# Performance work log

Hardware: AMD Instinct MI355X
Metric: run time of the kernel (lower is better)

## Reference

```python
import jax, jax.numpy as jnp
import numpy as np

D_MODEL = 768
N_HEADS = 4          # n_kv_heads
D_HEAD = 64          # d_model // n_heads = 768 // 12
DIM = N_HEADS * D_HEAD  # 256


def _feature_map(x):
    # ELU + 1 kernel approximation
    return jax.nn.elu(x) + 1.0


def setup_inputs() -> dict:
    key = jax.random.key(0)
    ks = jax.random.split(key, 6)
    B, T = 2, 4096
    s_in = 1.0 / np.sqrt(D_MODEL)
    s_out = 1.0 / np.sqrt(DIM)
    return {
        "x": jax.random.normal(ks[0], (B, T, D_MODEL), dtype=jnp.float32),
        "Wq": jax.random.normal(ks[1], (D_MODEL, DIM), dtype=jnp.float32) * s_in,
        "Wk": jax.random.normal(ks[2], (D_MODEL, DIM), dtype=jnp.float32) * s_in,
        "Wv": jax.random.normal(ks[3], (D_MODEL, DIM), dtype=jnp.float32) * s_in,
        "Wo": jax.random.normal(ks[4], (DIM, D_MODEL), dtype=jnp.float32) * s_out,
        "Wg": jax.random.normal(ks[5], (D_MODEL, D_MODEL), dtype=jnp.float32) * s_in,
    }


def reference(x, Wq, Wk, Wv, Wo, Wg):
    B, T, _ = x.shape
    H, D = N_HEADS, D_HEAD
    # projections -> (B, H, T, D)
    q = (x @ Wq).reshape(B, T, H, D).transpose(0, 2, 1, 3)
    k = (x @ Wk).reshape(B, T, H, D).transpose(0, 2, 1, 3)
    v = (x @ Wv).reshape(B, T, H, D).transpose(0, 2, 1, 3)
    q = _feature_map(q)
    k = _feature_map(k)
    # causal linear attention: running kv outer-product state, cumsum over T
    kv_cum = jnp.cumsum(jnp.einsum('bhte,bhtd->bhtde', k, v), axis=2)  # (B,H,T,D,D)
    z_cum = jnp.cumsum(k, axis=2)                                      # (B,H,T,D)
    out = jnp.einsum('bhte,bhted->bhtd', q, kv_cum)
    denom = jnp.maximum(jnp.einsum('bhte,bhte->bht', q, z_cum), 1e-6)[..., None]
    out = (out / denom).transpose(0, 2, 1, 3).reshape(B, T, H * D)
    gate = jax.nn.sigmoid(x @ Wg)
    return (out @ Wo) * gate
```

## Files before the change

kernel.cpp:

```cpp
#include <hip/hip_runtime.h>
#include <math.h>

#define BATCH 2
#define TSEQ 4096
#define DM 768
#define HEADS 4
#define DHEAD 64
#define DIMQ 256
#define MROWS (BATCH*TSEQ)
#define CHUNK 64
#define NCHUNK (TSEQ/CHUNK)
#define STATE (DHEAD*DHEAD + DHEAD)
#define KSPLIT (DM*2)
#define KS2 (DIMQ*2)

typedef __attribute__((ext_vector_type(8))) short bf16x8;
typedef __attribute__((ext_vector_type(4))) float f32x4;

__device__ __forceinline__ float act_elu1(float x){ return x > 0.f ? x + 1.f : expf(x); }
__device__ __forceinline__ float act_sig(float x){ return 1.f/(1.f + expf(-x)); }

__device__ __forceinline__ void fma4(float4& o, float a, const float4& b){
    o.x = fmaf(a, b.x, o.x); o.y = fmaf(a, b.y, o.y);
    o.z = fmaf(a, b.z, o.z); o.w = fmaf(a, b.w, o.w);
}
__device__ __forceinline__ float comp4(const float4& v, int u){
    return u==0 ? v.x : u==1 ? v.y : u==2 ? v.z : v.w;
}

__device__ __forceinline__ unsigned short bf16_rne(float f){
    unsigned u = __float_as_uint(f);
    u += 0x7FFFu + ((u >> 16) & 1u);
    return (unsigned short)(u >> 16);
}

__device__ __forceinline__ void gload_lds16(const void* g, void* l){
    __builtin_amdgcn_global_load_lds(
        (const __attribute__((address_space(1))) unsigned char*)g,
        (__attribute__((address_space(3))) unsigned char*)l, 16, 0, 0);
}

__global__ __launch_bounds__(192)
void split_x(const float* __restrict__ x, unsigned short* __restrict__ xs)
{
    const int r = blockIdx.x;
    const int c = threadIdx.x * 4;
    float4 v = *(const float4*)&x[(size_t)r*DM + c];
    float vv[4] = {v.x, v.y, v.z, v.w};
    unsigned short h[4], l[4];
    #pragma unroll
    for (int j = 0; j < 4; j++){
        h[j] = bf16_rne(vv[j]);
        float hf = __uint_as_float((unsigned)h[j] << 16);
        l[j] = bf16_rne(vv[j] - hf);
    }
    ushort4 h4 = {h[0],h[1],h[2],h[3]}, l4 = {l[0],l[1],l[2],l[3]};
    *(ushort4*)&xs[(size_t)r*KSPLIT + c] = h4;
    *(ushort4*)&xs[(size_t)r*KSPLIT + DM + c] = l4;
}

__global__ __launch_bounds__(256)
void split_w(const float* __restrict__ Wq, const float* __restrict__ Wk,
             const float* __restrict__ Wv, const float* __restrict__ Wg,
             unsigned short* __restrict__ wt)
{
    const int n0 = blockIdx.x * 64;
    const int k0 = blockIdx.y * 64;
    const float* W; int ldw, c0;
    if      (n0 < 256) { W = Wq; ldw = DIMQ; c0 = n0;       }
    else if (n0 < 512) { W = Wk; ldw = DIMQ; c0 = n0 - 256; }
    else if (n0 < 768) { W = Wv; ldw = DIMQ; c0 = n0 - 512; }
    else               { W = Wg; ldw = DM;   c0 = n0 - 768; }

    __shared__ float T[64][65];
    const int t = threadIdx.x;
    const int lr = t >> 4, lc = (t & 15) * 4;
    #pragma unroll
    for (int i = 0; i < 4; i++){
        int r = lr + i*16;
        float4 v = *(const float4*)&W[(size_t)(k0+r)*ldw + c0 + lc];
        T[r][lc+0]=v.x; T[r][lc+1]=v.y; T[r][lc+2]=v.z; T[r][lc+3]=v.w;
    }
    __syncthreads();
    const int rn = t >> 2, kc = (t & 3) * 16;
    unsigned short hb[16], lb[16];
    #pragma unroll
    for (int j = 0; j < 16; j++){
        float f = T[kc+j][rn];
        hb[j] = bf16_rne(f);
        float hf = __uint_as_float((unsigned)hb[j] << 16);
        lb[j] = bf16_rne(f - hf);
    }
    size_t base = (size_t)(n0+rn)*KSPLIT + k0 + kc;
    #pragma unroll
    for (int q = 0; q < 4; q++){
        ushort4 hv = {hb[q*4],hb[q*4+1],hb[q*4+2],hb[q*4+3]};
        ushort4 lv = {lb[q*4],lb[q*4+1],lb[q*4+2],lb[q*4+3]};
        *(ushort4*)&wt[base + q*4] = hv;
        *(ushort4*)&wt[base + DM + q*4] = lv;
    }
}

__global__ __launch_bounds__(256)
void split_wo(const float* __restrict__ Wo, unsigned short* __restrict__ wot)
{
    const int n0 = blockIdx.x * 64;
    const int k0 = blockIdx.y * 64;
    __shared__ float T[64][65];
    const int t = threadIdx.x;
    const int lr = t >> 4, lc = (t & 15) * 4;
    #pragma unroll
    for (int i = 0; i < 4; i++){
        int r = lr + i*16;
        float4 v = *(const float4*)&Wo[(size_t)(k0+r)*DM + n0 + lc];
        T[r][lc+0]=v.x; T[r][lc+1]=v.y; T[r][lc+2]=v.z; T[r][lc+3]=v.w;
    }
    __syncthreads();
    const int rn = t >> 2, kc = (t & 3) * 16;
    unsigned short hb[16], lb[16];
    #pragma unroll
    for (int j = 0; j < 16; j++){
        float f = T[kc+j][rn];
        hb[j] = bf16_rne(f);
        float hf = __uint_as_float((unsigned)hb[j] << 16);
        lb[j] = bf16_rne(f - hf);
    }
    size_t base = (size_t)(n0+rn)*KS2 + k0 + kc;
    #pragma unroll
    for (int q = 0; q < 4; q++){
        ushort4 hv = {hb[q*4],hb[q*4+1],hb[q*4+2],hb[q*4+3]};
        ushort4 lv = {lb[q*4],lb[q*4+1],lb[q*4+2],lb[q*4+3]};
        *(ushort4*)&wot[base + q*4] = hv;
        *(ushort4*)&wot[base + DIMQ + q*4] = lv;
    }
}

__global__ __launch_bounds__(256, 2)
void gemm_qkvg_mfma(const unsigned short* __restrict__ xs,
                    const unsigned short* __restrict__ wt,
                    float* __restrict__ qws, float* __restrict__ kws,
                    float* __restrict__ vws, float* __restrict__ gws)
{
    __shared__ unsigned short Ah[128*32];
    __shared__ unsigned short Al[128*32];
    __shared__ unsigned short Bh[128*32];
    __shared__ unsigned short Bl[128*32];

    const int m0 = blockIdx.x * 128;
    const int n0 = blockIdx.y * 128;
    const int tid = threadIdx.x;
    const int lane = tid & 63, w = tid >> 6;
    const int wm = (w & 1) * 64, wn = (w >> 1) * 64;
    const int l15 = lane & 15, lq = lane >> 4;

    const int srow = tid >> 2, scq = tid & 3;
    const unsigned short* xr0 = xs + (size_t)(m0+srow)   * KSPLIT + scq*8;
    const unsigned short* xr1 = xs + (size_t)(m0+srow+64)* KSPLIT + scq*8;
    const unsigned short* br0 = wt + (size_t)(n0+srow)   * KSPLIT + scq*8;
    const unsigned short* br1 = wt + (size_t)(n0+srow+64)* KSPLIT + scq*8;

    f32x4 acc[4][4];
    #pragma unroll
    for (int i = 0; i < 4; i++)
        #pragma unroll
        for (int j = 0; j < 4; j++)
            acc[i][j] = (f32x4){0.f, 0.f, 0.f, 0.f};

    #pragma unroll 1
    for (int ks = 0; ks < 24; ks++){
        const int o = ks*32;
        __syncthreads();
        gload_lds16(xr0 + o,      &Ah[tid*8]);
        gload_lds16(xr1 + o,      &Ah[2048 + tid*8]);
        gload_lds16(xr0 + DM + o, &Al[tid*8]);
        gload_lds16(xr1 + DM + o, &Al[2048 + tid*8]);
        gload_lds16(br0 + o,      &Bh[tid*8]);
        gload_lds16(br1 + o,      &Bh[2048 + tid*8]);
        gload_lds16(br0 + DM + o, &Bl[tid*8]);
        gload_lds16(br1 + DM + o, &Bl[2048 + tid*8]);
        __syncthreads();

        bf16x8 ah[4], al[4], bh[4], bl[4];
        #pragma unroll
        for (int im = 0; im < 4; im++){
            ah[im] = *(const bf16x8*)&Ah[(wm + im*16 + l15)*32 + lq*8];
            al[im] = *(const bf16x8*)&Al[(wm + im*16 + l15)*32 + lq*8];
        }
        #pragma unroll
        for (int jn = 0; jn < 4; jn++){
            bh[jn] = *(const bf16x8*)&Bh[(wn + jn*16 + l15)*32 + lq*8];
            bl[jn] = *(const bf16x8*)&Bl[(wn + jn*16 + l15)*32 + lq*8];
        }
        #pragma unroll
        for (int im = 0; im < 4; im++)
            #pragma unroll
            for (int jn = 0; jn < 4; jn++){
                acc[im][jn] = __builtin_amdgcn_mfma_f32_16x16x32_bf16(
                    ah[im], bh[jn], acc[im][jn], 0, 0, 0);
                acc[im][jn] = __builtin_amdgcn_mfma_f32_16x16x32_bf16(
                    ah[im], bl[jn], acc[im][jn], 0, 0, 0);
                acc[im][jn] = __builtin_amdgcn_mfma_f32_16x16x32_bf16(
                    al[im], bh[jn], acc[im][jn], 0, 0, 0);
            }
    }

    float* dst; int ld, cb, mode;
    const int bj = blockIdx.y;
    if      (bj < 2) { dst = qws; ld = DIMQ; cb = bj*128;       mode = 1; }
    else if (bj < 4) { dst = kws; ld = DIMQ; cb = (bj-2)*128;   mode = 1; }
    else if (bj < 6) { dst = vws; ld = DIMQ; cb = (bj-4)*128;   mode = 0; }
    else             { dst = gws; ld = DM;   cb = (bj-6)*128;   mode = 2; }

    #pragma unroll
    for (int im = 0; im < 4; im++){
        const int rb = m0 + wm + im*16 + lq*4;
        #pragma unroll
        for (int jn = 0; jn < 4; jn++){
            const int col = cb + wn + jn*16 + l15;
            f32x4 a = acc[im][jn];
            #pragma unroll
            for (int r = 0; r < 4; r++){
                float v0 = a[r];
                float vv = (mode == 1) ? act_elu1(v0)
                         : (mode == 2) ? act_sig(v0) : v0;
                dst[(size_t)(rb + r)*ld + col] = vv;
            }
        }
    }
}

__global__ __launch_bounds__(256, 2)
void chunk_state(const float* __restrict__ kws, const float* __restrict__ vws,
                 float* __restrict__ Sws)
{
    __shared__ float Ks[64][64];
    __shared__ float Vt[64][68];

    const int blk = blockIdx.x;
    const int c = blk & (NCHUNK-1);
    const int bh = blk >> 6;
    const int b = bh >> 2, h = bh & 3;
    const int row0 = b*TSEQ + c*CHUNK;
    const int col0 = h*DHEAD;
    const int tid = threadIdx.x;

    #pragma unroll
    for (int i = 0; i < 4; i++) {
        int flat = tid + i*256;
        int s = flat >> 4, dq = flat & 15;
        float4 k4 = *(const float4*)&kws[(size_t)(row0+s)*DIMQ + col0 + dq*4];
        *(float4*)&Ks[s][dq*4] = k4;
        float4 v4 = *(const float4*)&vws[(size_t)(row0+s)*DIMQ + col0 + dq*4];
        Vt[dq*4+0][s] = v4.x; Vt[dq*4+1][s] = v4.y;
        Vt[dq*4+2][s] = v4.z; Vt[dq*4+3][s] = v4.w;
    }
    __syncthreads();

    const int e = tid >> 2, d0 = (tid & 3) * 16;
    float acc[16];
    #pragma unroll
    for (int j = 0; j < 16; j++) acc[j] = 0.f;
    for (int s = 0; s < 64; s++) {
        float ve = Vt[e][s];
        #pragma unroll
        for (int j = 0; j < 16; j++) acc[j] = fmaf(ve, Ks[s][d0+j], acc[j]);
    }
    float* Sp = Sws + (size_t)blk * STATE;
    #pragma unroll
    for (int j = 0; j < 16; j++) Sp[e*64 + d0 + j] = acc[j];

    if (tid < 64) {
        float z = 0.f;
        for (int s = 0; s < 64; s++) z += Ks[s][tid];
        Sp[4096 + tid] = z;
    }
}

__global__ __launch_bounds__(256)
void prefix_scan(const float* __restrict__ Sws, float* __restrict__ Pws)
{
    const int bh = blockIdx.x;
    const int i = blockIdx.y*256 + threadIdx.x;
    if (i >= STATE) return;
    const size_t base = (size_t)bh * NCHUNK * STATE;
    float run = 0.f;
    const float* sp = Sws + base + i;
    float* pp = Pws + base + i;
    #pragma unroll 4
    for (int c = 0; c < NCHUNK; c++) {
        pp[(size_t)c * STATE] = run;
        run += sp[(size_t)c * STATE];
    }
}

__global__ __launch_bounds__(256, 2)
void chunk_out(const float* __restrict__ qws, const float* __restrict__ kws,
               const float* __restrict__ vws, const float* __restrict__ Pws,
               unsigned short* __restrict__ attn_s)
{
    __shared__ float Qs[64][68];
    __shared__ float Ks[64][64];
    __shared__ float VA[64][68];
    __shared__ float Ps[64][64];
    __shared__ float zP[64];
    __shared__ float dpart[64][4];
    __shared__ float dinv[64];

    const int blk = blockIdx.x;
    const int c = blk & (NCHUNK-1);
    const int bh = blk >> 6;
    const int b = bh >> 2, h = bh & 3;
    const int row0 = b*TSEQ + c*CHUNK;
    const int col0 = h*DHEAD;
    const int tid = threadIdx.x;
    const float* Pp = Pws + (size_t)blk * STATE;

    #pragma unroll
    for (int i = 0; i < 4; i++) {
        int flat = tid + i*256;
        int s = flat >> 4, dq = flat & 15;
        float4 q4 = *(const float4*)&qws[(size_t)(row0+s)*DIMQ + col0 + dq*4];
        Qs[s][dq*4+0] = q4.x; Qs[s][dq*4+1] = q4.y;
        Qs[s][dq*4+2] = q4.z; Qs[s][dq*4+3] = q4.w;
        float4 k4 = *(const float4*)&kws[(size_t)(row0+s)*DIMQ + col0 + dq*4];
        *(float4*)&Ks[s][dq*4] = k4;
        float4 v4 = *(const float4*)&vws[(size_t)(row0+s)*DIMQ + col0 + dq*4];
        VA[dq*4+0][s] = v4.x; VA[dq*4+1][s] = v4.y;
        VA[dq*4+2][s] = v4.z; VA[dq*4+3][s] = v4.w;
        float4 p4 = *(const float4*)&Pp[flat*4];
        *(float4*)&Ps[0][flat*4] = p4;
    }
    if (tid < 16) {
        *(float4*)&zP[tid*4] = *(const float4*)&Pp[4096 + tid*4];
    }
    __syncthreads();

    const int t  = tid >> 2;
    const int qq = tid & 3;
    const int s0 = qq * 16;

    float4 qreg[16];
    #pragma unroll
    for (int eq = 0; eq < 16; eq++) qreg[eq] = *(const float4*)&Qs[t][eq*4];

    float dsum = 0.f;
    for (int i = 0; i < 16; i++) {
        int s = s0 + i;
        if (s <= t) {
            float a = 0.f;
            #pragma unroll
            for (int eq = 0; eq < 16; eq++) {
                float4 k4 = *(const float4*)&Ks[s][eq*4];
                float4 qv = qreg[eq];
                a = fmaf(qv.x, k4.x, a); a = fmaf(qv.y, k4.y, a);
                a = fmaf(qv.z, k4.z, a); a = fmaf(qv.w, k4.w, a);
            }
            dsum += a;
        }
    }
    dpart[t][qq] = dsum;

    float areg[16];
    #pragma unroll
    for (int i = 0; i < 16; i++) areg[i] = 0.f;
    #pragma unroll
    for (int eq = 0; eq < 16; eq++) {
        float4 qv = qreg[eq];
        #pragma unroll
        for (int u = 0; u < 4; u++) {
            int e = eq*4 + u;
            float qe = comp4(qv, u);
            float4 v0 = *(const float4*)&VA[e][s0+0];
            float4 v1 = *(const float4*)&VA[e][s0+4];
            float4 v2 = *(const float4*)&VA[e][s0+8];
            float4 v3 = *(const float4*)&VA[e][s0+12];
            areg[0]=fmaf(qe,v0.x,areg[0]);  areg[1]=fmaf(qe,v0.y,areg[1]);
            areg[2]=fmaf(qe,v0.z,areg[2]);  areg[3]=fmaf(qe,v0.w,areg[3]);
            areg[4]=fmaf(qe,v1.x,areg[4]);  areg[5]=fmaf(qe,v1.y,areg[5]);
            areg[6]=fmaf(qe,v1.z,areg[6]);  areg[7]=fmaf(qe,v1.w,areg[7]);
            areg[8]=fmaf(qe,v2.x,areg[8]);  areg[9]=fmaf(qe,v2.y,areg[9]);
            areg[10]=fmaf(qe,v2.z,areg[10]); areg[11]=fmaf(qe,v2.w,areg[11]);
            areg[12]=fmaf(qe,v3.x,areg[12]); areg[13]=fmaf(qe,v3.y,areg[13]);
            areg[14]=fmaf(qe,v3.z,areg[14]); areg[15]=fmaf(qe,v3.w,areg[15]);
        }
    }
    __syncthreads();

    #pragma unroll
    for (int i4 = 0; i4 < 4; i4++) {
        float4 w;
        w.x = (s0 + i4*4 + 0 <= t) ? areg[i4*4+0] : 0.f;
        w.y = (s0 + i4*4 + 1 <= t) ? areg[i4*4+1] : 0.f;
        w.z = (s0 + i4*4 + 2 <= t) ? areg[i4*4+2] : 0.f;
        w.w = (s0 + i4*4 + 3 <= t) ? areg[i4*4+3] : 0.f;
        *(float4*)&VA[t][s0 + i4*4] = w;
    }
    if (qq == 0) {
        float den = dpart[t][0] + dpart[t][1] + dpart[t][2] + dpart[t][3];
        #pragma unroll
        for (int eq = 0; eq < 16; eq++) {
            float4 z4 = *(const float4*)&zP[eq*4];
            float4 qv = qreg[eq];
            den = fmaf(qv.x, z4.x, den); den = fmaf(qv.y, z4.y, den);
            den = fmaf(qv.z, z4.z, den); den = fmaf(qv.w, z4.w, den);
        }
        den = fmaxf(den, 1e-6f);
        dinv[t] = 1.f / den;
    }
    __syncthreads();

    const int d0 = qq * 16;
    float4 o0 = {0,0,0,0}, o1 = {0,0,0,0}, o2 = {0,0,0,0}, o3 = {0,0,0,0};
    #pragma unroll
    for (int eq = 0; eq < 16; eq++) {
        float4 qv = qreg[eq];
        #pragma unroll
        for (int u = 0; u < 4; u++) {
            int e = eq*4 + u;
            float qe = comp4(qv, u);
            fma4(o0, qe, *(const float4*)&Ps[e][d0+0]);
            fma4(o1, qe, *(const float4*)&Ps[e][d0+4]);
            fma4(o2, qe, *(const float4*)&Ps[e][d0+8]);
            fma4(o3, qe, *(const float4*)&Ps[e][d0+12]);
        }
    }
    for (int s = 0; s < 64; s++) {
        float a = VA[t][s];
        fma4(o0, a, *(const float4*)&Ks[s][d0+0]);
        fma4(o1, a, *(const float4*)&Ks[s][d0+4]);
        fma4(o2, a, *(const float4*)&Ks[s][d0+8]);
        fma4(o3, a, *(const float4*)&Ks[s][d0+12]);
    }
    float r = dinv[t];
    float vals[16] = {o0.x*r,o0.y*r,o0.z*r,o0.w*r, o1.x*r,o1.y*r,o1.z*r,o1.w*r,
                      o2.x*r,o2.y*r,o2.z*r,o2.w*r, o3.x*r,o3.y*r,o3.z*r,o3.w*r};
    unsigned short hv[16], lv[16];
    #pragma unroll
    for (int j = 0; j < 16; j++){
        hv[j] = bf16_rne(vals[j]);
        float hf = __uint_as_float((unsigned)hv[j] << 16);
        lv[j] = bf16_rne(vals[j] - hf);
    }
    unsigned short* ap = attn_s + (size_t)(row0+t)*KS2 + col0 + d0;
    #pragma unroll
    for (int q = 0; q < 4; q++){
        ushort4 h4 = {hv[q*4],hv[q*4+1],hv[q*4+2],hv[q*4+3]};
        ushort4 l4 = {lv[q*4],lv[q*4+1],lv[q*4+2],lv[q*4+3]};
        *(ushort4*)&ap[q*4] = h4;
        *(ushort4*)&ap[DIMQ + q*4] = l4;
    }
}

__global__ __launch_bounds__(256, 2)
void gemm_out_mfma(const unsigned short* __restrict__ attn_s,
                   const unsigned short* __restrict__ wot,
                   const float* __restrict__ gws, float* __restrict__ out)
{
    __shared__ unsigned short Ah[128*32];
    __shared__ unsigned short Al[128*32];
    __shared__ unsigned short Bh[128*32];
    __shared__ unsigned short Bl[128*32];

    const int m0 = blockIdx.x * 128;
    const int n0 = blockIdx.y * 128;
    const int tid = threadIdx.x;
    const int lane = tid & 63, w = tid >> 6;
    const int wm = (w & 1) * 64, wn = (w >> 1) * 64;
    const int l15 = lane & 15, lq = lane >> 4;

    const int srow = tid >> 2, scq = tid & 3;
    const unsigned short* ar0 = attn_s + (size_t)(m0+srow)   * KS2 + scq*8;
    const unsigned short* ar1 = attn_s + (size_t)(m0+srow+64)* KS2 + scq*8;
    const unsigned short* br0 = wot + (size_t)(n0+srow)   * KS2 + scq*8;
    const unsigned short* br1 = wot + (size_t)(n0+srow+64)* KS2 + scq*8;

    f32x4 acc[4][4];
    #pragma unroll
    for (int i = 0; i < 4; i++)
        #pragma unroll
        for (int j = 0; j < 4; j++)
            acc[i][j] = (f32x4){0.f, 0.f, 0.f, 0.f};

    #pragma unroll 1
    for (int ks = 0; ks < 8; ks++){
        const int o = ks*32;
        __syncthreads();
        gload_lds16(ar0 + o,        &Ah[tid*8]);
        gload_lds16(ar1 + o,        &Ah[2048 + tid*8]);
        gload_lds16(ar0 + DIMQ + o, &Al[tid*8]);
        gload_lds16(ar1 + DIMQ + o, &Al[2048 + tid*8]);
        gload_lds16(br0 + o,        &Bh[tid*8]);
        gload_lds16(br1 + o,        &Bh[2048 + tid*8]);
        gload_lds16(br0 + DIMQ + o, &Bl[tid*8]);
        gload_lds16(br1 + DIMQ + o, &Bl[2048 + tid*8]);
        __syncthreads();

        bf16x8 ah[4], al[4], bh[4], bl[4];
        #pragma unroll
        for (int im = 0; im < 4; im++){
            ah[im] = *(const bf16x8*)&Ah[(wm + im*16 + l15)*32 + lq*8];
            al[im] = *(const bf16x8*)&Al[(wm + im*16 + l15)*32 + lq*8];
        }
        #pragma unroll
        for (int jn = 0; jn < 4; jn++){
            bh[jn] = *(const bf16x8*)&Bh[(wn + jn*16 + l15)*32 + lq*8];
            bl[jn] = *(const bf16x8*)&Bl[(wn + jn*16 + l15)*32 + lq*8];
        }
        #pragma unroll
        for (int im = 0; im < 4; im++)
            #pragma unroll
            for (int jn = 0; jn < 4; jn++){
                acc[im][jn] = __builtin_amdgcn_mfma_f32_16x16x32_bf16(
                    ah[im], bh[jn], acc[im][jn], 0, 0, 0);
                acc[im][jn] = __builtin_amdgcn_mfma_f32_16x16x32_bf16(
                    ah[im], bl[jn], acc[im][jn], 0, 0, 0);
                acc[im][jn] = __builtin_amdgcn_mfma_f32_16x16x32_bf16(
                    al[im], bh[jn], acc[im][jn], 0, 0, 0);
            }
    }

    #pragma unroll
    for (int im = 0; im < 4; im++){
        const int rb = m0 + wm + im*16 + lq*4;
        #pragma unroll
        for (int jn = 0; jn < 4; jn++){
            const int col = n0 + wn + jn*16 + l15;
            f32x4 a = acc[im][jn];
            #pragma unroll
            for (int r = 0; r < 4; r++){
                size_t idx = (size_t)(rb + r)*DM + col;
                out[idx] = a[r] * gws[idx];
            }
        }
    }
}

extern "C" void kernel_launch(void* const* d_in, const int* in_sizes, int n_in,
                              void* d_out, int out_size, void* d_ws, size_t ws_size,
                              hipStream_t stream)
{
    const float* x  = (const float*)d_in[0];
    const float* Wq = (const float*)d_in[1];
    const float* Wk = (const float*)d_in[2];
    const float* Wv = (const float*)d_in[3];
    const float* Wo = (const float*)d_in[4];
    const float* Wg = (const float*)d_in[5];
    float* out = (float*)d_out;

    float* w    = (float*)d_ws;
    float* qws  = w;
    float* kws  = qws + (size_t)MROWS*DIMQ;
    float* vws  = kws + (size_t)MROWS*DIMQ;
    float* gws  = vws + (size_t)MROWS*DIMQ;
    float* region = gws + (size_t)MROWS*DM;
    unsigned short* xs = (unsigned short*)region;
    unsigned short* wt = xs + (size_t)MROWS*KSPLIT;
    float* Sws = region;
    float* Pws = Sws + (size_t)BATCH*HEADS*NCHUNK*STATE;
    unsigned short* attn_s = (unsigned short*)(Pws + (size_t)BATCH*HEADS*NCHUNK*STATE);
    unsigned short* wot = attn_s + (size_t)MROWS*KS2;

    hipLaunchKernelGGL(split_x, dim3(MROWS), dim3(192), 0, stream, x, xs);
    hipLaunchKernelGGL(split_w, dim3(24,12), dim3(256), 0, stream,
                       Wq, Wk, Wv, Wg, wt);
    hipLaunchKernelGGL(gemm_qkvg_mfma, dim3(64,12), dim3(256), 0, stream,
                       xs, wt, qws, kws, vws, gws);
    hipLaunchKernelGGL(split_wo, dim3(12,4), dim3(256), 0, stream, Wo, wot);
    hipLaunchKernelGGL(chunk_state, dim3(BATCH*HEADS*NCHUNK), dim3(256), 0, stream,
                       kws, vws, Sws);
    hipLaunchKernelGGL(prefix_scan, dim3(BATCH*HEADS, 17), dim3(256), 0, stream,
                       Sws, Pws);
    hipLaunchKernelGGL(chunk_out, dim3(BATCH*HEADS*NCHUNK), dim3(256), 0, stream,
                       qws, kws, vws, Pws, attn_s);
    hipLaunchKernelGGL(gemm_out_mfma, dim3(64,6), dim3(256), 0, stream,
                       attn_s, wot, gws, out);
}
```

Measured before the change: 224.6 us.

## Merge split kernels, vectorize chunk_state accumulators, retile output GEMM to 64x128

Fuses split_x and split_w into one prep launch to save a kernel launch. chunk_state now reads K rows and writes the state as float4 vectors instead of scalars. The output GEMM moves from 128x128 tiles with 4 waves to 64x128 tiles with 2 waves, doubling the grid to 768 blocks to raise occupancy across CUs. In exchange, each block gets less reuse of the Wo tile, and a quarter of the prep threads sit idle in the x-split blocks.

```diff
diff --git a/kernel.cpp b/kernel.cpp
--- a/kernel.cpp
+++ b/kernel.cpp
@@ -40,44 +40,48 @@
         (__attribute__((address_space(3))) unsigned char*)l, 16, 0, 0);
 }
 
-__global__ __launch_bounds__(192)
-void split_x(const float* __restrict__ x, unsigned short* __restrict__ xs)
-{
-    const int r = blockIdx.x;
-    const int c = threadIdx.x * 4;
-    float4 v = *(const float4*)&x[(size_t)r*DM + c];
-    float vv[4] = {v.x, v.y, v.z, v.w};
-    unsigned short h[4], l[4];
-    #pragma unroll
-    for (int j = 0; j < 4; j++){
-        h[j] = bf16_rne(vv[j]);
-        float hf = __uint_as_float((unsigned)h[j] << 16);
-        l[j] = bf16_rne(vv[j] - hf);
-    }
-    ushort4 h4 = {h[0],h[1],h[2],h[3]}, l4 = {l[0],l[1],l[2],l[3]};
-    *(ushort4*)&xs[(size_t)r*KSPLIT + c] = h4;
-    *(ushort4*)&xs[(size_t)r*KSPLIT + DM + c] = l4;
-}
-
 __global__ __launch_bounds__(256)
-void split_w(const float* __restrict__ Wq, const float* __restrict__ Wk,
-             const float* __restrict__ Wv, const float* __restrict__ Wg,
-             unsigned short* __restrict__ wt)
-{
-    const int n0 = blockIdx.x * 64;
-    const int k0 = blockIdx.y * 64;
+void prep(const float* __restrict__ x,
+          const float* __restrict__ Wq, const float* __restrict__ Wk,
+          const float* __restrict__ Wv, const float* __restrict__ Wg,
+          unsigned short* __restrict__ xs, unsigned short* __restrict__ wt)
+{
+    __shared__ float T[64][65];
+    const int bid = blockIdx.x;
+    const int t = threadIdx.x;
+
+    if (bid < MROWS) {
+        if (t < 192) {
+            const int r = bid;
+            const int c = t * 4;
+            float4 v = *(const float4*)&x[(size_t)r*DM + c];
+            float vv[4] = {v.x, v.y, v.z, v.w};
+            unsigned short h[4], l[4];
+            #pragma unroll
+            for (int j = 0; j < 4; j++){
+                h[j] = bf16_rne(vv[j]);
+                float hf = __uint_as_float((unsigned)h[j] << 16);
+                l[j] = bf16_rne(vv[j] - hf);
+            }
+            ushort4 h4 = {h[0],h[1],h[2],h[3]}, l4 = {l[0],l[1],l[2],l[3]};
+            *(ushort4*)&xs[(size_t)r*KSPLIT + c] = h4;
+            *(ushort4*)&xs[(size_t)r*KSPLIT + DM + c] = l4;
+        }
+        return;
+    }
+
+    const int i = bid - MROWS;
+    const int n0 = (i % 24)*64, k0 = (i / 24)*64;
     const float* W; int ldw, c0;
     if      (n0 < 256) { W = Wq; ldw = DIMQ; c0 = n0;       }
     else if (n0 < 512) { W = Wk; ldw = DIMQ; c0 = n0 - 256; }
     else if (n0 < 768) { W = Wv; ldw = DIMQ; c0 = n0 - 512; }
     else               { W = Wg; ldw = DM;   c0 = n0 - 768; }
 
-    __shared__ float T[64][65];
-    const int t = threadIdx.x;
     const int lr = t >> 4, lc = (t & 15) * 4;
     #pragma unroll
-    for (int i = 0; i < 4; i++){
-        int r = lr + i*16;
+    for (int ii = 0; ii < 4; ii++){
+        int r = lr + ii*16;
         float4 v = *(const float4*)&W[(size_t)(k0+r)*ldw + c0 + lc];
         T[r][lc+0]=v.x; T[r][lc+1]=v.y; T[r][lc+2]=v.z; T[r][lc+3]=v.w;
     }
@@ -257,17 +261,19 @@
     __syncthreads();
 
     const int e = tid >> 2, d0 = (tid & 3) * 16;
-    float acc[16];
-    #pragma unroll
-    for (int j = 0; j < 16; j++) acc[j] = 0.f;
+    float4 a0 = {0,0,0,0}, a1 = {0,0,0,0}, a2 = {0,0,0,0}, a3 = {0,0,0,0};
     for (int s = 0; s < 64; s++) {
         float ve = Vt[e][s];
-        #pragma unroll
-        for (int j = 0; j < 16; j++) acc[j] = fmaf(ve, Ks[s][d0+j], acc[j]);
+        fma4(a0, ve, *(const float4*)&Ks[s][d0+0]);
+        fma4(a1, ve, *(const float4*)&Ks[s][d0+4]);
+        fma4(a2, ve, *(const float4*)&Ks[s][d0+8]);
+        fma4(a3, ve, *(const float4*)&Ks[s][d0+12]);
     }
     float* Sp = Sws + (size_t)blk * STATE;
-    #pragma unroll
-    for (int j = 0; j < 16; j++) Sp[e*64 + d0 + j] = acc[j];
+    *(float4*)&Sp[e*64 + d0 + 0]  = a0;
+    *(float4*)&Sp[e*64 + d0 + 4]  = a1;
+    *(float4*)&Sp[e*64 + d0 + 8]  = a2;
+    *(float4*)&Sp[e*64 + d0 + 12] = a3;
 
     if (tid < 64) {
         float z = 0.f;
@@ -451,28 +457,37 @@
     }
 }
 
-__global__ __launch_bounds__(256, 2)
+__global__ __launch_bounds__(128, 2)
 void gemm_out_mfma(const unsigned short* __restrict__ attn_s,
                    const unsigned short* __restrict__ wot,
                    const float* __restrict__ gws, float* __restrict__ out)
 {
-    __shared__ unsigned short Ah[128*32];
-    __shared__ unsigned short Al[128*32];
+    __shared__ unsigned short Ah[64*32];
+    __shared__ unsigned short Al[64*32];
     __shared__ unsigned short Bh[128*32];
     __shared__ unsigned short Bl[128*32];
 
-    const int m0 = blockIdx.x * 128;
+    const int m0 = blockIdx.x * 64;
     const int n0 = blockIdx.y * 128;
     const int tid = threadIdx.x;
     const int lane = tid & 63, w = tid >> 6;
-    const int wm = (w & 1) * 64, wn = (w >> 1) * 64;
+    const int wn = w * 64;
     const int l15 = lane & 15, lq = lane >> 4;
 
-    const int srow = tid >> 2, scq = tid & 3;
-    const unsigned short* ar0 = attn_s + (size_t)(m0+srow)   * KS2 + scq*8;
-    const unsigned short* ar1 = attn_s + (size_t)(m0+srow+64)* KS2 + scq*8;
-    const unsigned short* br0 = wot + (size_t)(n0+srow)   * KS2 + scq*8;
-    const unsigned short* br1 = wot + (size_t)(n0+srow+64)* KS2 + scq*8;
+    const unsigned short* ap[2]; int ad[2];
+    #pragma unroll
+    for (int j = 0; j < 2; j++){
+        int f = w*128 + j*64 + lane;
+        ap[j] = attn_s + (size_t)(m0 + (f>>2))*KS2 + (f&3)*8;
+        ad[j] = f*8;
+    }
+    const unsigned short* bp[4]; int bd[4];
+    #pragma unroll
+    for (int j = 0; j < 4; j++){
+        int f = w*256 + j*64 + lane;
+        bp[j] = wot + (size_t)(n0 + (f>>2))*KS2 + (f&3)*8;
+        bd[j] = f*8;
+    }
 
     f32x4 acc[4][4];
     #pragma unroll
@@ -485,21 +500,23 @@
     for (int ks = 0; ks < 8; ks++){
         const int o = ks*32;
         __syncthreads();
-        gload_lds16(ar0 + o,        &Ah[tid*8]);
-        gload_lds16(ar1 + o,        &Ah[2048 + tid*8]);
-        gload_lds16(ar0 + DIMQ + o, &Al[tid*8]);
-        gload_lds16(ar1 + DIMQ + o, &Al[2048 + tid*8]);
-        gload_lds16(br0 + o,        &Bh[tid*8]);
-        gload_lds16(br1 + o,        &Bh[2048 + tid*8]);
-        gload_lds16(br0 + DIMQ + o, &Bl[tid*8]);
-        gload_lds16(br1 + DIMQ + o, &Bl[2048 + tid*8]);
+        #pragma unroll
+        for (int j = 0; j < 2; j++){
+            gload_lds16(ap[j] + o,        &Ah[ad[j]]);
+            gload_lds16(ap[j] + DIMQ + o, &Al[ad[j]]);
+        }
+        #pragma unroll
+        for (int j = 0; j < 4; j++){
+            gload_lds16(bp[j] + o,        &Bh[bd[j]]);
+            gload_lds16(bp[j] + DIMQ + o, &Bl[bd[j]]);
+        }
         __syncthreads();
 
         bf16x8 ah[4], al[4], bh[4], bl[4];
         #pragma unroll
         for (int im = 0; im < 4; im++){
-            ah[im] = *(const bf16x8*)&Ah[(wm + im*16 + l15)*32 + lq*8];
-            al[im] = *(const bf16x8*)&Al[(wm + im*16 + l15)*32 + lq*8];
+            ah[im] = *(const bf16x8*)&Ah[(im*16 + l15)*32 + lq*8];
+            al[im] = *(const bf16x8*)&Al[(im*16 + l15)*32 + lq*8];
         }
         #pragma unroll
         for (int jn = 0; jn < 4; jn++){
@@ -521,7 +538,7 @@
 
     #pragma unroll
     for (int im = 0; im < 4; im++){
-        const int rb = m0 + wm + im*16 + lq*4;
+        const int rb = m0 + im*16 + lq*4;
         #pragma unroll
         for (int jn = 0; jn < 4; jn++){
             const int col = n0 + wn + jn*16 + l15;
@@ -560,9 +577,8 @@
     unsigned short* attn_s = (unsigned short*)(Pws + (size_t)BATCH*HEADS*NCHUNK*STATE);
     unsigned short* wot = attn_s + (size_t)MROWS*KS2;
 
-    hipLaunchKernelGGL(split_x, dim3(MROWS), dim3(192), 0, stream, x, xs);
-    hipLaunchKernelGGL(split_w, dim3(24,12), dim3(256), 0, stream,
-                       Wq, Wk, Wv, Wg, wt);
+    hipLaunchKernelGGL(prep, dim3(MROWS + 288), dim3(256), 0, stream,
+                       x, Wq, Wk, Wv, Wg, xs, wt);
     hipLaunchKernelGGL(gemm_qkvg_mfma, dim3(64,12), dim3(256), 0, stream,
                        xs, wt, qws, kws, vws, gws);
     hipLaunchKernelGGL(split_wo, dim3(12,4), dim3(256), 0, stream, Wo, wot);
@@ -572,6 +588,6 @@
                        Sws, Pws);
     hipLaunchKernelGGL(chunk_out, dim3(BATCH*HEADS*NCHUNK), dim3(256), 0, stream,
                        qws, kws, vws, Pws, attn_s);
-    hipLaunchKernelGGL(gemm_out_mfma, dim3(64,6), dim3(256), 0, stream,
+    hipLaunchKernelGGL(gemm_out_mfma, dim3(128,6), dim3(128), 0, stream,
                        attn_s, wot, gws, out);
 }
```

Result: no change. 224.7 us (+0.0%).

## Merge prep kernels, vectorize chunk state, and use cumulative-K denominator in chunk_out

Applied to the files above, without the earlier changes.

Folds split_x and split_w into one prep launch and folds the Wo split into the chunk_state launch, cutting the number of kernel launches from eight to six. chunk_state accumulates and stores with float4. prefix_scan is re-gridded to one thread per state element, with all chunk loads issued before the running sum. chunk_out now computes the denominator from an in-block cumulative sum of K instead of the masked per-pair QK loop, and reuses the Ps buffer, padded to reduce LDS bank conflicts, for the prefix state. The cost is larger register arrays in the scan, a serial 64-step cumsum in chunk_out, and an extra barrier plus extra LDS traffic.

```diff
diff --git a/kernel.cpp b/kernel.cpp
--- a/kernel.cpp
+++ b/kernel.cpp
@@ -10,6 +10,7 @@
 #define MROWS (BATCH*TSEQ)
 #define CHUNK 64
 #define NCHUNK (TSEQ/CHUNK)
+#define NBH (BATCH*HEADS)
 #define STATE (DHEAD*DHEAD + DHEAD)
 #define KSPLIT (DM*2)
 #define KS2 (DIMQ*2)
@@ -40,44 +41,48 @@
         (__attribute__((address_space(3))) unsigned char*)l, 16, 0, 0);
 }
 
-__global__ __launch_bounds__(192)
-void split_x(const float* __restrict__ x, unsigned short* __restrict__ xs)
-{
-    const int r = blockIdx.x;
-    const int c = threadIdx.x * 4;
-    float4 v = *(const float4*)&x[(size_t)r*DM + c];
-    float vv[4] = {v.x, v.y, v.z, v.w};
-    unsigned short h[4], l[4];
-    #pragma unroll
-    for (int j = 0; j < 4; j++){
-        h[j] = bf16_rne(vv[j]);
-        float hf = __uint_as_float((unsigned)h[j] << 16);
-        l[j] = bf16_rne(vv[j] - hf);
-    }
-    ushort4 h4 = {h[0],h[1],h[2],h[3]}, l4 = {l[0],l[1],l[2],l[3]};
-    *(ushort4*)&xs[(size_t)r*KSPLIT + c] = h4;
-    *(ushort4*)&xs[(size_t)r*KSPLIT + DM + c] = l4;
-}
-
 __global__ __launch_bounds__(256)
-void split_w(const float* __restrict__ Wq, const float* __restrict__ Wk,
-             const float* __restrict__ Wv, const float* __restrict__ Wg,
-             unsigned short* __restrict__ wt)
-{
-    const int n0 = blockIdx.x * 64;
-    const int k0 = blockIdx.y * 64;
+void prep(const float* __restrict__ x,
+          const float* __restrict__ Wq, const float* __restrict__ Wk,
+          const float* __restrict__ Wv, const float* __restrict__ Wg,
+          unsigned short* __restrict__ xs, unsigned short* __restrict__ wt)
+{
+    __shared__ float T[64][65];
+    const int bid = blockIdx.x;
+    const int t = threadIdx.x;
+
+    if (bid < MROWS) {
+        if (t < 192) {
+            const int r = bid;
+            const int c = t * 4;
+            float4 v = *(const float4*)&x[(size_t)r*DM + c];
+            float vv[4] = {v.x, v.y, v.z, v.w};
+            unsigned short h[4], l[4];
+            #pragma unroll
+            for (int j = 0; j < 4; j++){
+                h[j] = bf16_rne(vv[j]);
+                float hf = __uint_as_float((unsigned)h[j] << 16);
+                l[j] = bf16_rne(vv[j] - hf);
+            }
+            ushort4 h4 = {h[0],h[1],h[2],h[3]}, l4 = {l[0],l[1],l[2],l[3]};
+            *(ushort4*)&xs[(size_t)r*KSPLIT + c] = h4;
+            *(ushort4*)&xs[(size_t)r*KSPLIT + DM + c] = l4;
+        }
+        return;
+    }
+
+    const int i = bid - MROWS;
+    const int n0 = (i % 24)*64, k0 = (i / 24)*64;
     const float* W; int ldw, c0;
     if      (n0 < 256) { W = Wq; ldw = DIMQ; c0 = n0;       }
     else if (n0 < 512) { W = Wk; ldw = DIMQ; c0 = n0 - 256; }
     else if (n0 < 768) { W = Wv; ldw = DIMQ; c0 = n0 - 512; }
     else               { W = Wg; ldw = DM;   c0 = n0 - 768; }
 
-    __shared__ float T[64][65];
-    const int t = threadIdx.x;
     const int lr = t >> 4, lc = (t & 15) * 4;
     #pragma unroll
-    for (int i = 0; i < 4; i++){
-        int r = lr + i*16;
+    for (int ii = 0; ii < 4; ii++){
+        int r = lr + ii*16;
         float4 v = *(const float4*)&W[(size_t)(k0+r)*ldw + c0 + lc];
         T[r][lc+0]=v.x; T[r][lc+1]=v.y; T[r][lc+2]=v.z; T[r][lc+3]=v.w;
     }
@@ -98,40 +103,6 @@
         ushort4 lv = {lb[q*4],lb[q*4+1],lb[q*4+2],lb[q*4+3]};
         *(ushort4*)&wt[base + q*4] = hv;
         *(ushort4*)&wt[base + DM + q*4] = lv;
-    }
-}
-
-__global__ __launch_bounds__(256)
-void split_wo(const float* __restrict__ Wo, unsigned short* __restrict__ wot)
-{
-    const int n0 = blockIdx.x * 64;
-    const int k0 = blockIdx.y * 64;
-    __shared__ float T[64][65];
-    const int t = threadIdx.x;
-    const int lr = t >> 4, lc = (t & 15) * 4;
-    #pragma unroll
-    for (int i = 0; i < 4; i++){
-        int r = lr + i*16;
-        float4 v = *(const float4*)&Wo[(size_t)(k0+r)*DM + n0 + lc];
-        T[r][lc+0]=v.x; T[r][lc+1]=v.y; T[r][lc+2]=v.z; T[r][lc+3]=v.w;
-    }
-    __syncthreads();
-    const int rn = t >> 2, kc = (t & 3) * 16;
-    unsigned short hb[16], lb[16];
-    #pragma unroll
-    for (int j = 0; j < 16; j++){
-        float f = T[kc+j][rn];
-        hb[j] = bf16_rne(f);
-        float hf = __uint_as_float((unsigned)hb[j] << 16);
-        lb[j] = bf16_rne(f - hf);
-    }
-    size_t base = (size_t)(n0+rn)*KS2 + k0 + kc;
-    #pragma unroll
-    for (int q = 0; q < 4; q++){
-        ushort4 hv = {hb[q*4],hb[q*4+1],hb[q*4+2],hb[q*4+3]};
-        ushort4 lv = {lb[q*4],lb[q*4+1],lb[q*4+2],lb[q*4+3]};
-        *(ushort4*)&wot[base + q*4] = hv;
-        *(ushort4*)&wot[base + DIMQ + q*4] = lv;
     }
 }
 
@@ -230,19 +201,53 @@
 }
 
 __global__ __launch_bounds__(256, 2)
-void chunk_state(const float* __restrict__ kws, const float* __restrict__ vws,
-                 float* __restrict__ Sws)
+void chunk_state_wo(const float* __restrict__ kws, const float* __restrict__ vws,
+                    float* __restrict__ Sws,
+                    const float* __restrict__ Wo, unsigned short* __restrict__ wot)
 {
     __shared__ float Ks[64][64];
     __shared__ float Vt[64][68];
+    __shared__ float T[64][65];
 
     const int blk = blockIdx.x;
+    const int tid = threadIdx.x;
+
+    if (blk >= NBH*NCHUNK) {
+        const int i = blk - NBH*NCHUNK;
+        const int n0 = (i % 12)*64, k0 = (i / 12)*64;
+        const int lr = tid >> 4, lc = (tid & 15) * 4;
+        #pragma unroll
+        for (int ii = 0; ii < 4; ii++){
+            int r = lr + ii*16;
+            float4 v = *(const float4*)&Wo[(size_t)(k0+r)*DM + n0 + lc];
+            T[r][lc+0]=v.x; T[r][lc+1]=v.y; T[r][lc+2]=v.z; T[r][lc+3]=v.w;
+        }
+        __syncthreads();
+        const int rn = tid >> 2, kc = (tid & 3) * 16;
+        unsigned short hb[16], lb[16];
+        #pragma unroll
+        for (int j = 0; j < 16; j++){
+            float f = T[kc+j][rn];
+            hb[j] = bf16_rne(f);
+            float hf = __uint_as_float((unsigned)hb[j] << 16);
+            lb[j] = bf16_rne(f - hf);
+        }
+        size_t base = (size_t)(n0+rn)*KS2 + k0 + kc;
+        #pragma unroll
+        for (int q = 0; q < 4; q++){
+            ushort4 hv = {hb[q*4],hb[q*4+1],hb[q*4+2],hb[q*4+3]};
+            ushort4 lv = {lb[q*4],lb[q*4+1],lb[q*4+2],lb[q*4+3]};
+            *(ushort4*)&wot[base + q*4] = hv;
+            *(ushort4*)&wot[base + DIMQ + q*4] = lv;
+        }
+        return;
+    }
+
     const int c = blk & (NCHUNK-1);
     const int bh = blk >> 6;
     const int b = bh >> 2, h = bh & 3;
     const int row0 = b*TSEQ + c*CHUNK;
     const int col0 = h*DHEAD;
-    const int tid = threadIdx.x;
 
     #pragma unroll
     for (int i = 0; i < 4; i++) {
@@ -257,17 +262,19 @@
     __syncthreads();
 
     const int e = tid >> 2, d0 = (tid & 3) * 16;
-    float acc[16];
-    #pragma unroll
-    for (int j = 0; j < 16; j++) acc[j] = 0.f;
+    float4 a0 = {0,0,0,0}, a1 = {0,0,0,0}, a2 = {0,0,0,0}, a3 = {0,0,0,0};
     for (int s = 0; s < 64; s++) {
         float ve = Vt[e][s];
-        #pragma unroll
-        for (int j = 0; j < 16; j++) acc[j] = fmaf(ve, Ks[s][d0+j], acc[j]);
+        fma4(a0, ve, *(const float4*)&Ks[s][d0+0]);
+        fma4(a1, ve, *(const float4*)&Ks[s][d0+4]);
+        fma4(a2, ve, *(const float4*)&Ks[s][d0+8]);
+        fma4(a3, ve, *(const float4*)&Ks[s][d0+12]);
     }
     float* Sp = Sws + (size_t)blk * STATE;
-    #pragma unroll
-    for (int j = 0; j < 16; j++) Sp[e*64 + d0 + j] = acc[j];
+    *(float4*)&Sp[e*64 + d0 + 0]  = a0;
+    *(float4*)&Sp[e*64 + d0 + 4]  = a1;
+    *(float4*)&Sp[e*64 + d0 + 8]  = a2;
+    *(float4*)&Sp[e*64 + d0 + 12] = a3;
 
     if (tid < 64) {
         float z = 0.f;
@@ -279,17 +286,21 @@
 __global__ __launch_bounds__(256)
 void prefix_scan(const float* __restrict__ Sws, float* __restrict__ Pws)
 {
-    const int bh = blockIdx.x;
-    const int i = blockIdx.y*256 + threadIdx.x;
-    if (i >= STATE) return;
-    const size_t base = (size_t)bh * NCHUNK * STATE;
+    const int colg = blockIdx.x*256 + threadIdx.x;
+    if (colg >= NBH*STATE) return;
+    const int bh = colg / STATE;
+    const int i = colg - bh*STATE;
+    const size_t base = (size_t)bh * NCHUNK * STATE + i;
+    const float* sp = Sws + base;
+    float* pp = Pws + base;
+    float v[NCHUNK];
+    #pragma unroll
+    for (int c = 0; c < NCHUNK; c++) v[c] = sp[(size_t)c * STATE];
     float run = 0.f;
-    const float* sp = Sws + base + i;
-    float* pp = Pws + base + i;
-    #pragma unroll 4
-    for (int c = 0; c < NCHUNK; c++) {
+    #pragma unroll
+    for (int c = 0; c < NCHUNK; c++){
         pp[(size_t)c * STATE] = run;
-        run += sp[(size_t)c * STATE];
+        run += v[c];
     }
 }
 
@@ -301,7 +312,7 @@
     __shared__ float Qs[64][68];
     __shared__ float Ks[64][64];
     __shared__ float VA[64][68];
-    __shared__ float Ps[64][64];
+    __shared__ float Ps[64][68];
     __shared__ float zP[64];
     __shared__ float dpart[64][4];
     __shared__ float dinv[64];
@@ -327,11 +338,16 @@
         float4 v4 = *(const float4*)&vws[(size_t)(row0+s)*DIMQ + col0 + dq*4];
         VA[dq*4+0][s] = v4.x; VA[dq*4+1][s] = v4.y;
         VA[dq*4+2][s] = v4.z; VA[dq*4+3][s] = v4.w;
-        float4 p4 = *(const float4*)&Pp[flat*4];
-        *(float4*)&Ps[0][flat*4] = p4;
-    }
-    if (tid < 16) {
-        *(float4*)&zP[tid*4] = *(const float4*)&Pp[4096 + tid*4];
+    }
+    __syncthreads();
+
+    if (tid < 64) {
+        float run = 0.f;
+        for (int s = 0; s < 64; s++){ run += Ks[s][tid]; Ps[s][tid] = run; }
+    }
+    if (tid >= 192 && tid < 208) {
+        int q = tid - 192;
+        *(float4*)&zP[q*4] = *(const float4*)&Pp[4096 + q*4];
     }
     __syncthreads();
 
@@ -343,22 +359,21 @@
     #pragma unroll
     for (int eq = 0; eq < 16; eq++) qreg[eq] = *(const float4*)&Qs[t][eq*4];
 
-    float dsum = 0.f;
-    for (int i = 0; i < 16; i++) {
-        int s = s0 + i;
-        if (s <= t) {
-            float a = 0.f;
-            #pragma unroll
-            for (int eq = 0; eq < 16; eq++) {
-                float4 k4 = *(const float4*)&Ks[s][eq*4];
-                float4 qv = qreg[eq];
-                a = fmaf(qv.x, k4.x, a); a = fmaf(qv.y, k4.y, a);
-                a = fmaf(qv.z, k4.z, a); a = fmaf(qv.w, k4.w, a);
-            }
-            dsum += a;
-        }
-    }
-    dpart[t][qq] = dsum;
+    {
+        float dsum = 0.f;
+        #pragma unroll
+        for (int j = 0; j < 4; j++){
+            int eq = qq*4 + j;
+            float4 qv = qreg[eq];
+            float4 kc = *(const float4*)&Ps[t][eq*4];
+            float4 z4 = *(const float4*)&zP[eq*4];
+            dsum = fmaf(qv.x, kc.x + z4.x, dsum);
+            dsum = fmaf(qv.y, kc.y + z4.y, dsum);
+            dsum = fmaf(qv.z, kc.z + z4.z, dsum);
+            dsum = fmaf(qv.w, kc.w + z4.w, dsum);
+        }
+        dpart[t][qq] = dsum;
+    }
 
     float areg[16];
     #pragma unroll
@@ -388,24 +403,23 @@
 
     #pragma unroll
     for (int i4 = 0; i4 < 4; i4++) {
-        float4 w;
-        w.x = (s0 + i4*4 + 0 <= t) ? areg[i4*4+0] : 0.f;
-        w.y = (s0 + i4*4 + 1 <= t) ? areg[i4*4+1] : 0.f;
-        w.z = (s0 + i4*4 + 2 <= t) ? areg[i4*4+2] : 0.f;
-        w.w = (s0 + i4*4 + 3 <= t) ? areg[i4*4+3] : 0.f;
-        *(float4*)&VA[t][s0 + i4*4] = w;
+        float4 wv;
+        wv.x = (s0 + i4*4 + 0 <= t) ? areg[i4*4+0] : 0.f;
+        wv.y = (s0 + i4*4 + 1 <= t) ? areg[i4*4+1] : 0.f;
+        wv.z = (s0 + i4*4 + 2 <= t) ? areg[i4*4+2] : 0.f;
+        wv.w = (s0 + i4*4 + 3 <= t) ? areg[i4*4+3] : 0.f;
+        *(float4*)&VA[t][s0 + i4*4] = wv;
     }
     if (qq == 0) {
         float den = dpart[t][0] + dpart[t][1] + dpart[t][2] + dpart[t][3];
-        #pragma unroll
-        for (int eq = 0; eq < 16; eq++) {
-            float4 z4 = *(const float4*)&zP[eq*4];
-            float4 qv = qreg[eq];
-            den = fmaf(qv.x, z4.x, den); den = fmaf(qv.y, z4.y, den);
-            den = fmaf(qv.z, z4.z, den); den = fmaf(qv.w, z4.w, den);
-        }
         den = fmaxf(den, 1e-6f);
         dinv[t] = 1.f / den;
+    }
+    #pragma unroll
+    for (int i = 0; i < 4; i++) {
+        int flat = (tid + i*256) * 4;
+        int e = flat >> 6, d = flat & 63;
+        *(float4*)&Ps[e][d] = *(const float4*)&Pp[flat];
     }
     __syncthreads();
 
@@ -441,13 +455,13 @@
         float hf = __uint_as_float((unsigned)hv[j] << 16);
         lv[j] = bf16_rne(vals[j] - hf);
     }
-    unsigned short* ap = attn_s + (size_t)(row0+t)*KS2 + col0 + d0;
+    unsigned short* apw = attn_s + (size_t)(row0+t)*KS2 + col0 + d0;
     #pragma unroll
     for (int q = 0; q < 4; q++){
         ushort4 h4 = {hv[q*4],hv[q*4+1],hv[q*4+2],hv[q*4+3]};
         ushort4 l4 = {lv[q*4],lv[q*4+1],lv[q*4+2],lv[q*4+3]};
-        *(ushort4*)&ap[q*4] = h4;
-        *(ushort4*)&ap[DIMQ + q*4] = l4;
+        *(ushort4*)&apw[q*4] = h4;
+        *(ushort4*)&apw[DIMQ + q*4] = l4;
     }
 }
 
@@ -556,21 +570,19 @@
     unsigned short* xs = (unsigned short*)region;
     unsigned short* wt = xs + (size_t)MROWS*KSPLIT;
     float* Sws = region;
-    float* Pws = Sws + (size_t)BATCH*HEADS*NCHUNK*STATE;
-    unsigned short* attn_s = (unsigned short*)(Pws + (size_t)BATCH*HEADS*NCHUNK*STATE);
+    float* Pws = Sws + (size_t)NBH*NCHUNK*STATE;
+    unsigned short* attn_s = (unsigned short*)(Pws + (size_t)NBH*NCHUNK*STATE);
     unsigned short* wot = attn_s + (size_t)MROWS*KS2;
 
-    hipLaunchKernelGGL(split_x, dim3(MROWS), dim3(192), 0, stream, x, xs);
-    hipLaunchKernelGGL(split_w, dim3(24,12), dim3(256), 0, stream,
-                       Wq, Wk, Wv, Wg, wt);
+    hipLaunchKernelGGL(prep, dim3(MROWS + 288), dim3(256), 0, stream,
+                       x, Wq, Wk, Wv, Wg, xs, wt);
     hipLaunchKernelGGL(gemm_qkvg_mfma, dim3(64,12), dim3(256), 0, stream,
                        xs, wt, qws, kws, vws, gws);
-    hipLaunchKernelGGL(split_wo, dim3(12,4), dim3(256), 0, stream, Wo, wot);
-    hipLaunchKernelGGL(chunk_state, dim3(BATCH*HEADS*NCHUNK), dim3(256), 0, stream,
-                       kws, vws, Sws);
-    hipLaunchKernelGGL(prefix_scan, dim3(BATCH*HEADS, 17), dim3(256), 0, stream,
+    hipLaunchKernelGGL(chunk_state_wo, dim3(NBH*NCHUNK + 48), dim3(256), 0, stream,
+                       kws, vws, Sws, Wo, wot);
+    hipLaunchKernelGGL(prefix_scan, dim3((NBH*STATE + 255)/256), dim3(256), 0, stream,
                        Sws, Pws);
-    hipLaunchKernelGGL(chunk_out, dim3(BATCH*HEADS*NCHUNK), dim3(256), 0, stream,
+    hipLaunchKernelGGL(chunk_out, dim3(NBH*NCHUNK), dim3(256), 0, stream,
                        qws, kws, vws, Pws, attn_s);
     hipLaunchKernelGGL(gemm_out_mfma, dim3(64,6), dim3(256), 0, stream,
                        attn_s, wot, gws, out);
```

After: 215.8 us. 1.04x faster.
